# Optimization experiments

Hardware: AMD Instinct MI355X
Metric: run time of the kernel (lower is better)

The kernel has to match this reference:

```python
import jax, jax.numpy as jnp
import numpy as np

OUT = 2048          # rows of sparse weight (out_features)
IN = 2048           # cols of sparse weight (in_features)
NNZ_PER_ROW = 128   # uniform nnz per row -> simple valid CSR indptr
NNZ = OUT * NNZ_PER_ROW
N = 512             # number of input rows (tokens)


def setup_inputs() -> dict:
    key = jax.random.key(0)
    k1, k2, k3 = jax.random.split(key, 3)
    x = jax.random.normal(k1, (N, IN), dtype=jnp.float32)
    data = jax.random.normal(k2, (NNZ,), dtype=jnp.float32)
    # sorted column indices per row (canonical-ish CSR; duplicates are harmless, they sum)
    indices = jnp.sort(
        jax.random.randint(k3, (OUT, NNZ_PER_ROW), 0, IN), axis=1
    ).reshape(NNZ).astype(jnp.int32)
    indptr = (jnp.arange(OUT + 1) * NNZ_PER_ROW).astype(jnp.int32)
    return {"x": x, "data": data, "indices": indices, "indptr": indptr}


def reference(x, data, indices, indptr):
    # CuPyLinear.forward: result = (W_csr @ x.T).T, i.e. y = x @ W.T with W sparse CSR.
    nnz = data.shape[0]
    n_rows = indptr.shape[0] - 1  # static
    # expand CSR indptr to per-nnz row ids
    rows = jnp.searchsorted(indptr, jnp.arange(nnz, dtype=indptr.dtype), side="right") - 1
    # contrib[k, n] = data[k] * x[n, col[k]]
    contrib = data[:, None] * x.T[indices]                 # [nnz, N]
    y_t = jax.ops.segment_sum(contrib, rows, num_segments=n_rows)  # [out, N]
    return y_t.T                                           # [N, out]
```

## Files before the change

kernel.cpp:

```cpp
#include <hip/hip_runtime.h>

#define N_TOK 512
#define IN_F  2048
#define OUT_F 2048
#define NNZ_ROW 128

#define TTOK 8
#define NTILE (N_TOK / TTOK)

#define ROWS 64
#define TPB  32
#define TILES_PB (TPB / TTOK)
#define WPITCH 132
#define YPITCH 36

#define SW_BYTES (ROWS * WPITCH * 4)
#define SX_BYTES (IN_F * TTOK * 2)
#define SY_BYTES (ROWS * YPITCH * 4)
#define SMEM_BYTES (SW_BYTES + SX_BYTES + SY_BYTES)

__device__ ushort g_xt[NTILE * IN_F * TTOK];

static __device__ __forceinline__ unsigned f2bf(float f) {
    unsigned u = __float_as_uint(f);
    return (u + 0x7fffu + ((u >> 16) & 1u)) >> 16;
}

__global__ __launch_bounds__(256) void tile_x(const float* __restrict__ x) {
    const int tile = blockIdx.y;
    const int c    = blockIdx.x * 256 + threadIdx.x;
    unsigned o[4];
#pragma unroll
    for (int j = 0; j < 4; ++j) {
        const float a = x[(tile * TTOK + 2 * j    ) * IN_F + c];
        const float b = x[(tile * TTOK + 2 * j + 1) * IN_F + c];
        o[j] = f2bf(a) | (f2bf(b) << 16);
    }
    ((uint4*)g_xt)[tile * IN_F + c] = make_uint4(o[0], o[1], o[2], o[3]);
}

__global__ __launch_bounds__(256, 2) void spmm(const float* __restrict__ data,
                                               const int*   __restrict__ indices,
                                               const int*   __restrict__ indptr,
                                               float*       __restrict__ y) {
    extern __shared__ unsigned smem[];
    unsigned* s_w = smem;
    ushort*   s_x = (ushort*)((char*)smem + SW_BYTES);
    float*    s_y = (float*)((char*)smem + SW_BYTES + SX_BYTES);

    const int rg = blockIdx.x;
    const int tb = blockIdx.y;
    const int r0 = rg * ROWS;
    const int t  = threadIdx.x;

    const int base0 = indptr[r0];
    const int4*   I4 = (const int4*)(indices + base0);
    const float4* D4 = (const float4*)(data + base0);
#pragma unroll
    for (int i = 0; i < (ROWS * NNZ_ROW / 4) / 256; ++i) {
        const int    e  = t + i * 256;
        const int4   ci = I4[e];
        const float4 dv = D4[e];
        const int    r  = e >> 5;
        const int    k0 = (e & 31) * 4;
        unsigned* dst = &s_w[r * WPITCH + k0];
        dst[0] = (__float_as_uint(dv.x) & 0xFFFFF800u) | (unsigned)ci.x;
        dst[1] = (__float_as_uint(dv.y) & 0xFFFFF800u) | (unsigned)ci.y;
        dst[2] = (__float_as_uint(dv.z) & 0xFFFFF800u) | (unsigned)ci.z;
        dst[3] = (__float_as_uint(dv.w) & 0xFFFFF800u) | (unsigned)ci.w;
    }

    const int l  = t & 63;
    const int w  = t >> 6;
    const int rw = w * 16 + (l >> 2);
    const int q  = (l >> 1) & 1;
    const int kh = l & 1;
    const unsigned* wrow = &s_w[rw * WPITCH];
    const uint2* sx2 = (const uint2*)s_x;

    for (int ti = 0; ti < TILES_PB; ++ti) {
        const char* src = (const char*)g_xt +
                          (size_t)(tb * TILES_PB + ti) * SX_BYTES;
#pragma unroll
        for (int i = 0; i < (SX_BYTES / 16) / 256; ++i) {
            const int off = (t + i * 256) * 16;
            __builtin_amdgcn_global_load_lds((const unsigned*)(src + off),
                                             (unsigned*)((char*)s_x + off),
                                             16, 0, 0);
        }
        __syncthreads();

        float4 acc = make_float4(0.f, 0.f, 0.f, 0.f);
#pragma unroll 8
        for (int j = 0; j < NNZ_ROW / 2; ++j) {
            const unsigned u  = wrow[2 * j + kh];
            const float    wt = __uint_as_float(u & 0xFFFFF800u);
            const uint2    xv = sx2[(u & 2047u) * 2 + q];
            acc.x += wt * __uint_as_float(xv.x << 16);
            acc.y += wt * __uint_as_float(xv.x);
            acc.z += wt * __uint_as_float(xv.y << 16);
            acc.w += wt * __uint_as_float(xv.y);
        }
        acc.x += __shfl_xor(acc.x, 1);
        acc.y += __shfl_xor(acc.y, 1);
        acc.z += __shfl_xor(acc.z, 1);
        acc.w += __shfl_xor(acc.w, 1);
        if (kh == 0)
            *(float4*)&s_y[rw * YPITCH + ti * TTOK + q * 4] = acc;
        __syncthreads();
    }

    const int n  = t >> 3;
    const int rb = t & 7;
    float v[8];
#pragma unroll
    for (int j = 0; j < 8; ++j) v[j] = s_y[(rb * 8 + j) * YPITCH + n];
    float* yp = &y[(size_t)(tb * TPB + n) * OUT_F + r0 + rb * 8];
    *(float4*)yp       = make_float4(v[0], v[1], v[2], v[3]);
    *((float4*)yp + 1) = make_float4(v[4], v[5], v[6], v[7]);
}

extern "C" void kernel_launch(void* const* d_in, const int* in_sizes, int n_in,
                              void* d_out, int out_size, void* d_ws, size_t ws_size,
                              hipStream_t stream) {
    const float* x       = (const float*)d_in[0];
    const float* data    = (const float*)d_in[1];
    const int*   indices = (const int*)  d_in[2];
    const int*   indptr  = (const int*)  d_in[3];
    float*       y       = (float*)d_out;

    tile_x<<<dim3(IN_F / 256, NTILE), 256, 0, stream>>>(x);
    spmm<<<dim3(OUT_F / ROWS, N_TOK / TPB), 256, SMEM_BYTES, stream>>>(
        data, indices, indptr, y);
}
```

Baseline: 79.41 us.

## Double-buffer x tiles in LDS and split each row's nnz across four lanes

Token tiles shrink from 8 to 4, so each LDS x tile is half the size. Two x buffers are kept so the async global-to-LDS load of the next tile overlaps compute on the current one. The packed weight/index rows are stored as four strided chunks, with the pitch-33 spacing meant to reduce LDS bank conflicts. Four lanes now split a row's nnz and combine through two shuffle stages. The cost is twice as many tile iterations and barriers, plus more LDS per block from the second x buffer.

```diff
diff --git a/kernel.cpp b/kernel.cpp
--- a/kernel.cpp
+++ b/kernel.cpp
@@ -5,7 +5,7 @@
 #define OUT_F 2048
 #define NNZ_ROW 128
 
-#define TTOK 8
+#define TTOK 4
 #define NTILE (N_TOK / TTOK)
 
 #define ROWS 64
@@ -14,10 +14,12 @@
 #define WPITCH 132
 #define YPITCH 36
 
+#define SX_BYTES (IN_F * TTOK * 2)
+#define SW_OFF   (2 * SX_BYTES)
 #define SW_BYTES (ROWS * WPITCH * 4)
-#define SX_BYTES (IN_F * TTOK * 2)
+#define SY_OFF   (SW_OFF + SW_BYTES)
 #define SY_BYTES (ROWS * YPITCH * 4)
-#define SMEM_BYTES (SW_BYTES + SX_BYTES + SY_BYTES)
+#define SMEM_BYTES (SY_OFF + SY_BYTES)
 
 __device__ ushort g_xt[NTILE * IN_F * TTOK];
 
@@ -29,24 +31,22 @@
 __global__ __launch_bounds__(256) void tile_x(const float* __restrict__ x) {
     const int tile = blockIdx.y;
     const int c    = blockIdx.x * 256 + threadIdx.x;
-    unsigned o[4];
-#pragma unroll
-    for (int j = 0; j < 4; ++j) {
-        const float a = x[(tile * TTOK + 2 * j    ) * IN_F + c];
-        const float b = x[(tile * TTOK + 2 * j + 1) * IN_F + c];
-        o[j] = f2bf(a) | (f2bf(b) << 16);
-    }
-    ((uint4*)g_xt)[tile * IN_F + c] = make_uint4(o[0], o[1], o[2], o[3]);
+    const unsigned lo = f2bf(x[(tile * TTOK + 0) * IN_F + c]) |
+                        (f2bf(x[(tile * TTOK + 1) * IN_F + c]) << 16);
+    const unsigned hi = f2bf(x[(tile * TTOK + 2) * IN_F + c]) |
+                        (f2bf(x[(tile * TTOK + 3) * IN_F + c]) << 16);
+    ((uint2*)g_xt)[tile * IN_F + c] = make_uint2(lo, hi);
 }
 
 __global__ __launch_bounds__(256, 2) void spmm(const float* __restrict__ data,
                                                const int*   __restrict__ indices,
                                                const int*   __restrict__ indptr,
                                                float*       __restrict__ y) {
-    extern __shared__ unsigned smem[];
-    unsigned* s_w = smem;
-    ushort*   s_x = (ushort*)((char*)smem + SW_BYTES);
-    float*    s_y = (float*)((char*)smem + SW_BYTES + SX_BYTES);
+    extern __shared__ char smem[];
+    ushort*   s_x0 = (ushort*)smem;
+    ushort*   s_x1 = (ushort*)(smem + SX_BYTES);
+    unsigned* s_w  = (unsigned*)(smem + SW_OFF);
+    float*    s_y  = (float*)(smem + SY_OFF);
 
     const int rg = blockIdx.x;
     const int tb = blockIdx.y;
@@ -62,51 +62,57 @@
         const int4   ci = I4[e];
         const float4 dv = D4[e];
         const int    r  = e >> 5;
-        const int    k0 = (e & 31) * 4;
-        unsigned* dst = &s_w[r * WPITCH + k0];
-        dst[0] = (__float_as_uint(dv.x) & 0xFFFFF800u) | (unsigned)ci.x;
-        dst[1] = (__float_as_uint(dv.y) & 0xFFFFF800u) | (unsigned)ci.y;
-        dst[2] = (__float_as_uint(dv.z) & 0xFFFFF800u) | (unsigned)ci.z;
-        dst[3] = (__float_as_uint(dv.w) & 0xFFFFF800u) | (unsigned)ci.w;
+        const int    m  = e & 31;
+        unsigned* dst = s_w + r * WPITCH + m;
+        dst[0]  = (__float_as_uint(dv.x) & 0xFFFFF800u) | (unsigned)ci.x;
+        dst[33] = (__float_as_uint(dv.y) & 0xFFFFF800u) | (unsigned)ci.y;
+        dst[66] = (__float_as_uint(dv.z) & 0xFFFFF800u) | (unsigned)ci.z;
+        dst[99] = (__float_as_uint(dv.w) & 0xFFFFF800u) | (unsigned)ci.w;
     }
+
+    auto STAGE_X = [&](ushort* buf, int tile) {
+        const char* src = (const char*)g_xt + (size_t)tile * SX_BYTES;
+#pragma unroll
+        for (int i = 0; i < (SX_BYTES / 16) / 256; ++i) {
+            const int off = (t + i * 256) * 16;
+            __builtin_amdgcn_global_load_lds((const unsigned*)(src + off),
+                                             (unsigned*)((char*)buf + off),
+                                             16, 0, 0);
+        }
+    };
 
     const int l  = t & 63;
     const int w  = t >> 6;
     const int rw = w * 16 + (l >> 2);
-    const int q  = (l >> 1) & 1;
-    const int kh = l & 1;
-    const unsigned* wrow = &s_w[rw * WPITCH];
-    const uint2* sx2 = (const uint2*)s_x;
+    const int kh = l & 3;
+    const unsigned* wrow = s_w + rw * WPITCH + kh * 33;
+
+    STAGE_X(s_x0, tb * TILES_PB);
+    __syncthreads();
 
     for (int ti = 0; ti < TILES_PB; ++ti) {
-        const char* src = (const char*)g_xt +
-                          (size_t)(tb * TILES_PB + ti) * SX_BYTES;
-#pragma unroll
-        for (int i = 0; i < (SX_BYTES / 16) / 256; ++i) {
-            const int off = (t + i * 256) * 16;
-            __builtin_amdgcn_global_load_lds((const unsigned*)(src + off),
-                                             (unsigned*)((char*)s_x + off),
-                                             16, 0, 0);
-        }
-        __syncthreads();
+        ushort* cur = (ti & 1) ? s_x1 : s_x0;
+        ushort* nxt = (ti & 1) ? s_x0 : s_x1;
+        if (ti + 1 < TILES_PB) STAGE_X(nxt, tb * TILES_PB + ti + 1);
 
+        const uint2* sx = (const uint2*)cur;
         float4 acc = make_float4(0.f, 0.f, 0.f, 0.f);
 #pragma unroll 8
-        for (int j = 0; j < NNZ_ROW / 2; ++j) {
-            const unsigned u  = wrow[2 * j + kh];
+        for (int j = 0; j < NNZ_ROW / 4; ++j) {
+            const unsigned u  = wrow[j];
             const float    wt = __uint_as_float(u & 0xFFFFF800u);
-            const uint2    xv = sx2[(u & 2047u) * 2 + q];
+            const uint2    xv = sx[u & 2047u];
             acc.x += wt * __uint_as_float(xv.x << 16);
             acc.y += wt * __uint_as_float(xv.x);
             acc.z += wt * __uint_as_float(xv.y << 16);
             acc.w += wt * __uint_as_float(xv.y);
         }
-        acc.x += __shfl_xor(acc.x, 1);
-        acc.y += __shfl_xor(acc.y, 1);
-        acc.z += __shfl_xor(acc.z, 1);
-        acc.w += __shfl_xor(acc.w, 1);
+        acc.x += __shfl_xor(acc.x, 1); acc.y += __shfl_xor(acc.y, 1);
+        acc.z += __shfl_xor(acc.z, 1); acc.w += __shfl_xor(acc.w, 1);
+        acc.x += __shfl_xor(acc.x, 2); acc.y += __shfl_xor(acc.y, 2);
+        acc.z += __shfl_xor(acc.z, 2); acc.w += __shfl_xor(acc.w, 2);
         if (kh == 0)
-            *(float4*)&s_y[rw * YPITCH + ti * TTOK + q * 4] = acc;
+            *(float4*)&s_y[rw * YPITCH + ti * TTOK] = acc;
         __syncthreads();
     }
 
```

New measurement: 81.01 us, median of 2. 1.02x slower.
